# Performance work log

Measured on AMD Instinct MI355X. Metric: run time of the kernel, lower is better.

The kernel has to match this reference:

```python
import jax, jax.numpy as jnp
import numpy as np
from jax import lax

B, C, H, W = 8, 384, 32, 32
HEADS, G, STRIDE, KSIZE = 12, 6, 2, 3
HC = C // HEADS          # head channels = 32
CG = C // G              # group channels = 64
NGH = HEADS // G         # heads per group = 2
DEPTHS = 2
D2 = C * 4               # MLP hidden
HK, WK = H // STRIDE, W // STRIDE
NS = HK * WK             # deformable samples = 256
SCALE = HC ** -0.5


def dwconv(x, w, b, stride=1, pad=1):
    # depthwise conv, x:(N,Cx,H,W), w:(Cx,kh,kw)
    c = x.shape[1]
    y = lax.conv_general_dilated(x, w[:, None], (stride, stride),
                                 [(pad, pad), (pad, pad)], feature_group_count=c,
                                 dimension_numbers=('NCHW', 'OIHW', 'NCHW'))
    return y + b[None, :, None, None]


def conv1x1(x, w, b=None):
    y = jnp.einsum('oc,bchw->bohw', w, x)
    return y if b is None else y + b[None, :, None, None]


def layernorm_c(x, w, b, eps=1e-5):
    # LayerNormProxy: LN over channel dim of NCHW
    xt = x.transpose(0, 2, 3, 1)
    mu = xt.mean(-1, keepdims=True)
    var = xt.var(-1, keepdims=True)
    xt = (xt - mu) * lax.rsqrt(var + eps) * w + b
    return xt.transpose(0, 3, 1, 2)


def grid_sample(img, grid):
    # F.grid_sample, bilinear, align_corners=True. img:(N,Ci,Hi,Wi), grid:(N,Hg,Wg,2) as (x,y) in [-1,1]
    N, Ci, Hi, Wi = img.shape
    gx = (grid[..., 0] + 1.0) * 0.5 * (Wi - 1)
    gy = (grid[..., 1] + 1.0) * 0.5 * (Hi - 1)
    x0 = jnp.floor(gx)
    y0 = jnp.floor(gy)
    wx = (gx - x0)[:, None]   # (N,1,Hg,Wg)
    wy = (gy - y0)[:, None]
    x0i = jnp.clip(x0.astype(jnp.int32), 0, Wi - 1)
    y0i = jnp.clip(y0.astype(jnp.int32), 0, Hi - 1)
    x1i = jnp.clip(x0i + 1, 0, Wi - 1)
    y1i = jnp.clip(y0i + 1, 0, Hi - 1)
    gather = jax.vmap(lambda im, yi, xi: im[:, yi, xi])  # -> (N,Ci,Hg,Wg)
    v00 = gather(img, y0i, x0i)
    v01 = gather(img, y0i, x1i)
    v10 = gather(img, y1i, x0i)
    v11 = gather(img, y1i, x1i)
    return (v00 * (1 - wx) * (1 - wy) + v01 * wx * (1 - wy)
            + v10 * (1 - wx) * wy + v11 * wx * wy)


def _norm_grid(hs, ws, centered):
    if centered:  # _get_ref_points
        ys = jnp.linspace(0.5, hs - 0.5, hs)
        xs = jnp.linspace(0.5, ws - 0.5, ws)
    else:         # _get_q_grid
        ys = jnp.arange(hs, dtype=jnp.float32)
        xs = jnp.arange(ws, dtype=jnp.float32)
    ys = ys / (hs - 1.0) * 2.0 - 1.0
    xs = xs / (ws - 1.0) * 2.0 - 1.0
    return jnp.stack(jnp.meshgrid(ys, xs, indexing='ij'), -1)  # (hs,ws,2) (y,x)


def dattn(x, wq, bq, wk, bk, wv, bv, wo, bo, odw, odb, olw, olb, opw, rpe):
    q = conv1x1(x, wq, bq)                              # (B,C,H,W)
    q_off = q.reshape(B * G, CG, H, W)
    off = dwconv(q_off, odw, odb, stride=STRIDE, pad=KSIZE // 2)  # (BG,CG,HK,WK)
    off = jax.nn.gelu(layernorm_c(off, olw, olb), approximate=False)
    off = conv1x1(off, opw).transpose(0, 2, 3, 1)       # (BG,HK,WK,2) as (dy,dx)
    ref = _norm_grid(HK, WK, True)[None]
    pos = jnp.clip(off + ref, -1.0, 1.0)                # (BG,HK,WK,2) (y,x)
    xs = grid_sample(x.reshape(B * G, CG, H, W), pos[..., ::-1])  # (BG,CG,HK,WK)
    xs = xs.reshape(B, C, 1, NS)
    qf = q.reshape(B * HEADS, HC, H * W)
    k = conv1x1(xs, wk, bk).reshape(B * HEADS, HC, NS)
    v = conv1x1(xs, wv, bv).reshape(B * HEADS, HC, NS)
    attn = jnp.einsum('bcm,bcn->bmn', qf, k) * SCALE    # (B*HEADS, HW, NS)
    rpe_g = jnp.broadcast_to(rpe[None], (B,) + rpe.shape).reshape(B * G, NGH, 2 * H - 1, 2 * W - 1)
    qg = _norm_grid(H, W, False).reshape(1, H * W, 2)
    disp = (qg[:, :, None, :] - pos.reshape(B * G, 1, NS, 2)) * 0.5  # (BG,HW,NS,2)
    bias = grid_sample(rpe_g, disp[..., ::-1]).reshape(B * HEADS, H * W, NS)
    attn = jax.nn.softmax(attn + bias, axis=2)
    out = jnp.einsum('bmn,bcn->bcm', attn, v).reshape(B, C, H, W)
    return conv1x1(out, wo, bo)


def _forward(x, lpu_w, lpu_b, wq, bq, wk, bk, wv, bv, wo, bo,
             off_dw_w, off_dw_b, off_ln_w, off_ln_b, off_pw_w, rpe,
             mlp_w1, mlp_b1, mlp_dw_w, mlp_dw_b, mlp_w2, mlp_b2):
    # proj is Identity (dim_in == dim_embed); layer_norms/layer_scales/drop_path are Identity; dropouts are 0
    for d in range(DEPTHS):
        x = x + dwconv(x, lpu_w[d], lpu_b[d])  # local perception unit
        x = x + dattn(x, wq[d], bq[d], wk[d], bk[d], wv[d], bv[d], wo[d], bo[d],
                      off_dw_w[d], off_dw_b[d], off_ln_w[d], off_ln_b[d], off_pw_w[d], rpe[d])
        h = conv1x1(x, mlp_w1[d], mlp_b1[d])
        h = h + dwconv(h, mlp_dw_w[d], mlp_dw_b[d])
        h = jax.nn.gelu(h, approximate=False)
        x = x + conv1x1(h, mlp_w2[d], mlp_b2[d])
    return x


def setup_inputs():
    key = jax.random.key(0)
    ks = iter(jax.random.split(key, 16))
    def p(shape, std=0.02):
        return jax.random.normal(next(ks), shape, jnp.float32) * std
    D = DEPTHS
    return {
        "x": jax.random.normal(next(ks), (B, C, H, W), jnp.float32),
        "lpu_w": p((D, C, 3, 3)), "lpu_b": jnp.zeros((D, C), jnp.float32),
        "wq": p((D, C, C)), "bq": jnp.zeros((D, C), jnp.float32),
        "wk": p((D, C, C)), "bk": jnp.zeros((D, C), jnp.float32),
        "wv": p((D, C, C)), "bv": jnp.zeros((D, C), jnp.float32),
        "wo": p((D, C, C)), "bo": jnp.zeros((D, C), jnp.float32),
        "off_dw_w": p((D, CG, 3, 3)), "off_dw_b": jnp.zeros((D, CG), jnp.float32),
        "off_ln_w": jnp.ones((D, CG), jnp.float32), "off_ln_b": jnp.zeros((D, CG), jnp.float32),
        "off_pw_w": p((D, 2, CG)),
        "rpe": p((D, HEADS, 2 * H - 1, 2 * W - 1), 0.01),
        "mlp_w1": p((D, D2, C)), "mlp_b1": jnp.zeros((D, D2), jnp.float32),
        "mlp_dw_w": p((D, D2, 3, 3)), "mlp_dw_b": jnp.zeros((D, D2), jnp.float32),
        "mlp_w2": p((D, C, D2)), "mlp_b2": jnp.zeros((D, C), jnp.float32),
    }


def reference(x, lpu_w, lpu_b, wq, bq, wk, bk, wv, bv, wo, bo,
              off_dw_w, off_dw_b, off_ln_w, off_ln_b, off_pw_w, rpe,
              mlp_w1, mlp_b1, mlp_dw_w, mlp_dw_b, mlp_w2, mlp_b2):
    return _forward(x, lpu_w, lpu_b, wq, bq, wk, bk, wv, bv, wo, bo,
                    off_dw_w, off_dw_b, off_ln_w, off_ln_b, off_pw_w, rpe,
                    mlp_w1, mlp_b1, mlp_dw_w, mlp_dw_b, mlp_w2, mlp_b2)
```

## Files before the change

kernel.cpp:

```cpp
#include <hip/hip_runtime.h>
#include <hip/hip_bf16.h>
#include <math.h>

namespace {

constexpr int B_ = 8, C_ = 384, H_ = 32, W_ = 32, HW_ = 1024;
constexpr int HEADS_ = 12, G_ = 6, HC_ = 32, CG_ = 64, NS_ = 256, D2_ = 1536;
constexpr float SCALE_ = 0.17677669529663687f;

using short8 = __attribute__((ext_vector_type(8))) short;
using f32x4 = __attribute__((ext_vector_type(4))) float;
using u32x4 = __attribute__((ext_vector_type(4))) unsigned;
typedef unsigned short ushort_t;

__device__ __forceinline__ float gelu_exact(float x) {
  return 0.5f * x * (1.f + erff(x * 0.70710678118654752f));
}
__device__ __forceinline__ ushort_t f2bf(float f) {
  unsigned u = __float_as_uint(f);
  u = (u + 0x7FFFu + ((u >> 16) & 1u)) >> 16;
  return (ushort_t)u;
}
__device__ __forceinline__ float bf2f(ushort_t s) {
  return __uint_as_float(((unsigned)s) << 16);
}
__device__ __forceinline__ float bflo(unsigned u) { return __uint_as_float(u << 16); }
__device__ __forceinline__ float bfhi(unsigned u) { return __uint_as_float(u & 0xFFFF0000u); }
__device__ __forceinline__ unsigned pack2(float a, float b) {
  return (unsigned)f2bf(a) | ((unsigned)f2bf(b) << 16);
}

typedef __attribute__((address_space(1))) const unsigned int gq_u32;
typedef __attribute__((address_space(3))) unsigned int lq_u32;
__device__ __forceinline__ void gload16(const ushort_t* g, ushort_t* l) {
  __builtin_amdgcn_global_load_lds((gq_u32*)g, (lq_u32*)l, 16, 0, 0);
}

__global__ __launch_bounds__(256) void wcvt_kernel(
    const float* __restrict__ s0, const float* __restrict__ s1,
    const float* __restrict__ s2, const float* __restrict__ s3,
    const float* __restrict__ s4, const float* __restrict__ s5,
    ushort_t* __restrict__ dst) {
  long idx = (long)blockIdx.x * 256 + threadIdx.x;
  long off = idx;
  const float* s;
  if (off < 294912) s = s0;
  else if ((off -= 294912) < 294912) s = s1;
  else if ((off -= 294912) < 294912) s = s2;
  else if ((off -= 294912) < 294912) s = s3;
  else if ((off -= 294912) < 1179648) s = s4;
  else { off -= 1179648; s = s5; }
  dst[idx] = f2bf(s[off]);
}

__global__ __launch_bounds__(256) void rpe_pack(const float* __restrict__ rpe,
                                               uint2* __restrict__ rpq) {
  int h = blockIdx.x, d = blockIdx.y;
  const float* rph = rpe + ((size_t)d * HEADS_ + h) * 3969;
  uint2* dst = rpq + ((size_t)d * HEADS_ + h) * 4096;
  for (int i = threadIdx.x; i < 4096; i += 256) {
    int y = i >> 6, x = i & 63;
    float v00 = 0.f, v01 = 0.f, v10 = 0.f, v11 = 0.f;
    if (y < 63) {
      if (x < 63) v00 = rph[y * 63 + x];
      if (x < 62) v01 = rph[y * 63 + x + 1];
    }
    if (y < 62) {
      if (x < 63) v10 = rph[(y + 1) * 63 + x];
      if (x < 62) v11 = rph[(y + 1) * 63 + x + 1];
    }
    dst[i] = make_uint2(pack2(v00, v01), pack2(v10, v11));
  }
}

__global__ __launch_bounds__(256) void dwconv_lpu(
    const float* __restrict__ x, const float* __restrict__ w,
    const float* __restrict__ bias, float* __restrict__ y,
    ushort_t* __restrict__ yt) {
  __shared__ __align__(16) float tile[32][33];
  int hp = blockIdx.x, c0 = blockIdx.y * 32, b = blockIdx.z;
  int t = threadIdx.x;
  int cl = t >> 3, g4 = t & 7;
  int c = c0 + cl;
  const float* img = x + ((size_t)b * C_ + c) * HW_;
  const float* wc = w + c * 9;
  float o0 = bias[c], o1 = o0, o2 = o0, o3 = o0;
#pragma unroll
  for (int ky = 0; ky < 3; ++ky) {
    int ih = hp + ky - 1;
    if ((unsigned)ih >= 32u) continue;
    const float* row = img + ih * 32 + g4 * 4;
    float4 m = *(const float4*)row;
    float v0 = (g4 > 0) ? row[-1] : 0.f;
    float v5 = (g4 < 7) ? row[4] : 0.f;
    float k0 = wc[ky * 3], k1 = wc[ky * 3 + 1], k2 = wc[ky * 3 + 2];
    o0 = fmaf(k0, v0, fmaf(k1, m.x, fmaf(k2, m.y, o0)));
    o1 = fmaf(k0, m.x, fmaf(k1, m.y, fmaf(k2, m.z, o1)));
    o2 = fmaf(k0, m.y, fmaf(k1, m.z, fmaf(k2, m.w, o2)));
    o3 = fmaf(k0, m.z, fmaf(k1, m.w, fmaf(k2, v5, o3)));
  }
  float4 ctr = *(const float4*)(img + hp * 32 + g4 * 4);
  o0 += ctr.x; o1 += ctr.y; o2 += ctr.z; o3 += ctr.w;
  *(float4*)(y + ((size_t)b * C_ + c) * HW_ + hp * 32 + g4 * 4) =
      make_float4(o0, o1, o2, o3);
  tile[cl][g4 * 4 + 0] = o0;
  tile[cl][g4 * 4 + 1] = o1;
  tile[cl][g4 * 4 + 2] = o2;
  tile[cl][g4 * 4 + 3] = o3;
  __syncthreads();
  int wl = t >> 3, cg = t & 7;
  unsigned p0 = pack2(tile[cg * 4 + 0][wl], tile[cg * 4 + 1][wl]);
  unsigned p1 = pack2(tile[cg * 4 + 2][wl], tile[cg * 4 + 3][wl]);
  unsigned* dst = (unsigned*)(yt + ((size_t)b * HW_ + hp * 32 + wl) * C_ + c0 + cg * 4);
  dst[0] = p0;
  dst[1] = p1;
}

__global__ __launch_bounds__(256) void dwgelu_t(
    const ushort_t* __restrict__ hin, const float* __restrict__ w,
    const float* __restrict__ bias, ushort_t* __restrict__ ht) {
  __shared__ __align__(16) float tile[2][32][33];
  int hp0 = blockIdx.x * 2, c0 = blockIdx.y * 32, b = blockIdx.z;
  int t = threadIdx.x;
  int cl = t >> 3, rw = (t >> 2) & 1, g8 = t & 3;
  int hp = hp0 + rw;
  int c = c0 + cl;
  const ushort_t* img = hin + ((size_t)b * D2_ + c) * HW_;
  const float* wc = w + c * 9;
  float o[8];
  float bi = bias[c];
#pragma unroll
  for (int j = 0; j < 8; ++j) o[j] = bi;
#pragma unroll
  for (int ky = 0; ky < 3; ++ky) {
    int ih = hp + ky - 1;
    if ((unsigned)ih >= 32u) continue;
    const ushort_t* row = img + ih * 32 + g8 * 8;
    uint4 u = *(const uint4*)row;
    float vv[10];
    vv[0] = (g8 > 0) ? bf2f(row[-1]) : 0.f;
    vv[1] = bflo(u.x); vv[2] = bfhi(u.x); vv[3] = bflo(u.y); vv[4] = bfhi(u.y);
    vv[5] = bflo(u.z); vv[6] = bfhi(u.z); vv[7] = bflo(u.w); vv[8] = bfhi(u.w);
    vv[9] = (g8 < 3) ? bf2f(row[8]) : 0.f;
    float k0 = wc[ky * 3], k1 = wc[ky * 3 + 1], k2 = wc[ky * 3 + 2];
#pragma unroll
    for (int j = 0; j < 8; ++j)
      o[j] = fmaf(k0, vv[j], fmaf(k1, vv[j + 1], fmaf(k2, vv[j + 2], o[j])));
  }
  {
    uint4 u = *(const uint4*)(img + hp * 32 + g8 * 8);
    float cv[8] = {bflo(u.x), bfhi(u.x), bflo(u.y), bfhi(u.y),
                   bflo(u.z), bfhi(u.z), bflo(u.w), bfhi(u.w)};
#pragma unroll
    for (int j = 0; j < 8; ++j) {
      o[j] += cv[j];
      tile[rw][cl][g8 * 8 + j] = gelu_exact(o[j]);
    }
  }
  __syncthreads();
  int wl = t >> 3, cg = t & 7;
#pragma unroll
  for (int rr = 0; rr < 2; ++rr) {
    unsigned p0 = pack2(tile[rr][cg * 4 + 0][wl], tile[rr][cg * 4 + 1][wl]);
    unsigned p1 = pack2(tile[rr][cg * 4 + 2][wl], tile[rr][cg * 4 + 3][wl]);
    unsigned* dst = (unsigned*)(ht + ((size_t)b * HW_ + (hp0 + rr) * 32 + wl) * D2_ + c0 + cg * 4);
    dst[0] = p0;
    dst[1] = p1;
  }
}

__global__ __launch_bounds__(256) void gemm_kv(
    const ushort_t* __restrict__ Wk, const ushort_t* __restrict__ Wv,
    const ushort_t* __restrict__ Xt, const float* __restrict__ bk,
    const float* __restrict__ bv, ushort_t* __restrict__ ktb,
    ushort_t* __restrict__ vbn) {
  constexpr int K = C_, N = NS_, O = C_;
  struct __align__(16) SMem {
    union {
      struct { char a[8192]; char b[8192]; } st;
      float shuf[64 * 68];
    };
  };
  __shared__ SMem sm;
  int t = threadIdx.x;
  int lane = t & 63, wave = t >> 6;
  int wm = (wave >> 1) * 32, wn = (wave & 1) * 32;
  int bz = blockIdx.z;
  bool isK = blockIdx.y < 6;
  int o0 = (isK ? blockIdx.y : blockIdx.y - 6) * 64;
  int n0 = blockIdx.x * 64;
  const ushort_t* Wb = isK ? Wk : Wv;
  const float* bias = isK ? bk : bv;
  const ushort_t* Ag = Wb + (size_t)o0 * K;
  const ushort_t* Bg = Xt + ((size_t)bz * N + n0) * K;
  int sr = t >> 3, sc = t & 7;
  int swz = ((sc ^ (sr & 7)) << 4);
  f32x4 acc[2][2];
#pragma unroll
  for (int fi = 0; fi < 2; ++fi)
#pragma unroll
    for (int fj = 0; fj < 2; ++fj) acc[fi][fj] = f32x4{0.f, 0.f, 0.f, 0.f};
  int lrow = lane & 15, lk = lane >> 4;
  short8 a0 = *(const short8*)(Ag + (size_t)sr * K + sc * 8);
  short8 a1 = *(const short8*)(Ag + (size_t)(sr + 32) * K + sc * 8);
  short8 b0 = *(const short8*)(Bg + (size_t)sr * K + sc * 8);
  short8 b1 = *(const short8*)(Bg + (size_t)(sr + 32) * K + sc * 8);
  constexpr int NSTEP = K / 64;
#pragma unroll
  for (int s = 0; s < NSTEP; ++s) {
    if (s) __syncthreads();
    *(short8*)(sm.st.a + sr * 128 + swz) = a0;
    *(short8*)(sm.st.a + (sr + 32) * 128 + swz) = a1;
    *(short8*)(sm.st.b + sr * 128 + swz) = b0;
    *(short8*)(sm.st.b + (sr + 32) * 128 + swz) = b1;
    __syncthreads();
    if (s + 1 < NSTEP) {
      int k0 = (s + 1) * 64;
      a0 = *(const short8*)(Ag + (size_t)sr * K + k0 + sc * 8);
      a1 = *(const short8*)(Ag + (size_t)(sr + 32) * K + k0 + sc * 8);
      b0 = *(const short8*)(Bg + (size_t)sr * K + k0 + sc * 8);
      b1 = *(const short8*)(Bg + (size_t)(sr + 32) * K + k0 + sc * 8);
    }
#pragma unroll
    for (int kk = 0; kk < 2; ++kk) {
      short8 af[2], bfr[2];
#pragma unroll
      for (int fi = 0; fi < 2; ++fi) {
        int row = wm + fi * 16 + lrow;
        af[fi] = *(const short8*)(sm.st.a + row * 128 + (((kk * 4 + lk) ^ (row & 7)) << 4));
      }
#pragma unroll
      for (int fj = 0; fj < 2; ++fj) {
        int row = wn + fj * 16 + lrow;
        bfr[fj] = *(const short8*)(sm.st.b + row * 128 + (((kk * 4 + lk) ^ (row & 7)) << 4));
      }
#pragma unroll
      for (int fi = 0; fi < 2; ++fi)
#pragma unroll
        for (int fj = 0; fj < 2; ++fj)
          acc[fi][fj] = __builtin_amdgcn_mfma_f32_16x16x32_bf16(af[fi], bfr[fj], acc[fi][fj], 0, 0, 0);
    }
  }
  __syncthreads();
#pragma unroll
  for (int fi = 0; fi < 2; ++fi) {
#pragma unroll
    for (int r = 0; r < 4; ++r) {
      int ol = wm + fi * 16 + lk * 4 + r;
      float bi = bias[o0 + ol];
#pragma unroll
      for (int fj = 0; fj < 2; ++fj) {
        int nl = wn + fj * 16 + lrow;
        sm.shuf[ol * 68 + nl] = acc[fi][fj][r] + bi;
      }
    }
  }
  __syncthreads();
  if (isK) {
    int nl = t >> 2, og = (t & 3) * 16;
    unsigned pk[8];
#pragma unroll
    for (int i = 0; i < 8; ++i)
      pk[i] = pack2(sm.shuf[(og + 2 * i) * 68 + nl], sm.shuf[(og + 2 * i + 1) * 68 + nl]);
    unsigned* dst = (unsigned*)(ktb + ((size_t)bz * N + (n0 + nl)) * O + o0 + og);
    *(uint4*)(dst) = make_uint4(pk[0], pk[1], pk[2], pk[3]);
    *(uint4*)(dst + 4) = make_uint4(pk[4], pk[5], pk[6], pk[7]);
  } else {
    int ol = t >> 2, ng = (t & 3) * 16;
    unsigned pk[8];
#pragma unroll
    for (int i = 0; i < 8; ++i)
      pk[i] = pack2(sm.shuf[ol * 68 + ng + 2 * i], sm.shuf[ol * 68 + ng + 2 * i + 1]);
    unsigned* dst = (unsigned*)(vbn + ((size_t)bz * O + (o0 + ol)) * N + n0 + ng);
    *(uint4*)(dst) = make_uint4(pk[0], pk[1], pk[2], pk[3]);
    *(uint4*)(dst + 4) = make_uint4(pk[4], pk[5], pk[6], pk[7]);
  }
}

template <bool F32, bool B16N, bool B16T, bool RES>
__global__ __launch_bounds__(256) void gemm128(
    const ushort_t* __restrict__ Wb, const ushort_t* __restrict__ Xt,
    const float* __restrict__ bias, const float* __restrict__ resid,
    float* __restrict__ Y, ushort_t* __restrict__ Yb, int O, int K, int N) {
  __shared__ __align__(16) ushort_t sA[2][128 * 64];
  __shared__ __align__(16) ushort_t sB[2][128 * 64];
  int t = threadIdx.x;
  int l = t & 63, w = t >> 6;
  int o0 = blockIdx.y * 128, n0 = blockIdx.x * 128, bz = blockIdx.z;
  const ushort_t* Ag = Wb + (size_t)o0 * K;
  const ushort_t* Bg = Xt + ((size_t)bz * N + n0) * K;
  int srow = w * 32 + (l >> 3);
  int scol = (l & 7) * 8;
  int lrow = l & 15, lg = l >> 4;
  int wm = (w >> 1) * 64, wn = (w & 1) * 64;
  f32x4 acc[4][4];
#pragma unroll
  for (int fi = 0; fi < 4; ++fi)
#pragma unroll
    for (int fj = 0; fj < 4; ++fj) acc[fi][fj] = f32x4{0.f, 0.f, 0.f, 0.f};
  auto stage = [&](int buf, int k0) {
#pragma unroll
    for (int i = 0; i < 4; ++i) {
      gload16(Ag + (size_t)(srow + i * 8) * K + k0 + scol, sA[buf] + (w * 32 + i * 8) * 64);
      gload16(Bg + (size_t)(srow + i * 8) * K + k0 + scol, sB[buf] + (w * 32 + i * 8) * 64);
    }
  };
  stage(0, 0);
  __syncthreads();
  int nstep = K >> 6;
  for (int s = 0; s < nstep; ++s) {
    int cur = s & 1;
    if (s + 1 < nstep) stage(cur ^ 1, (s + 1) * 64);
#pragma unroll
    for (int kk = 0; kk < 2; ++kk) {
      short8 af[4], bfr[4];
#pragma unroll
      for (int fi = 0; fi < 4; ++fi)
        af[fi] = *(const short8*)(sA[cur] + (wm + fi * 16 + lrow) * 64 + kk * 32 + lg * 8);
#pragma unroll
      for (int fj = 0; fj < 4; ++fj)
        bfr[fj] = *(const short8*)(sB[cur] + (wn + fj * 16 + lrow) * 64 + kk * 32 + lg * 8);
#pragma unroll
      for (int fi = 0; fi < 4; ++fi)
#pragma unroll
        for (int fj = 0; fj < 4; ++fj)
          acc[fi][fj] = __builtin_amdgcn_mfma_f32_16x16x32_bf16(af[fi], bfr[fj], acc[fi][fj], 0, 0, 0);
    }
    __syncthreads();
  }
#pragma unroll
  for (int fi = 0; fi < 4; ++fi) {
    int ob = wm + fi * 16 + lg * 4;
    float bi[4];
#pragma unroll
    for (int r = 0; r < 4; ++r) bi[r] = bias[o0 + ob + r];
#pragma unroll
    for (int fj = 0; fj < 4; ++fj) {
      int n = n0 + wn + fj * 16 + lrow;
      float v[4];
#pragma unroll
      for (int r = 0; r < 4; ++r) {
        v[r] = acc[fi][fj][r] + bi[r];
        if (RES) v[r] += resid[((size_t)bz * O + ob + r + o0) * N + n];
        if (F32) Y[((size_t)bz * O + ob + r + o0) * N + n] = v[r];
        if (B16N) Yb[((size_t)bz * O + ob + r + o0) * N + n] = f2bf(v[r]);
      }
      if (B16T) {
        uint2 u;
        u.x = pack2(v[0], v[1]);
        u.y = pack2(v[2], v[3]);
        *(uint2*)&Yb[((size_t)bz * N + n) * O + o0 + ob] = u;
      }
    }
  }
}

__global__ __launch_bounds__(256) void offset_kernel(
    const ushort_t* __restrict__ qt, const float* __restrict__ odw,
    const float* __restrict__ odb, const float* __restrict__ olw,
    const float* __restrict__ olb, const float* __restrict__ opw,
    float* __restrict__ pos) {
  int bg = blockIdx.x;
  int b = bg / G_, g = bg % G_;
  int t = threadIdx.x;
  int hk = t >> 4, wk = t & 15;
  const ushort_t* qb = qt + (size_t)b * HW_ * C_ + g * CG_;
  float sv[CG_];
#pragma unroll
  for (int cc = 0; cc < 8; ++cc) {
    float a8[8];
#pragma unroll
    for (int j = 0; j < 8; ++j) a8[j] = odb[cc * 8 + j];
#pragma unroll
    for (int ky = 0; ky < 3; ++ky) {
      int ih = 2 * hk + ky - 1;
      if ((unsigned)ih >= 32u) continue;
#pragma unroll
      for (int kx = 0; kx < 3; ++kx) {
        int iw = 2 * wk + kx - 1;
        if ((unsigned)iw >= 32u) continue;
        uint4 u = *(const uint4*)(qb + (size_t)(ih * 32 + iw) * C_ + cc * 8);
        float vv[8] = {bflo(u.x), bfhi(u.x), bflo(u.y), bfhi(u.y),
                       bflo(u.z), bfhi(u.z), bflo(u.w), bfhi(u.w)};
#pragma unroll
        for (int j = 0; j < 8; ++j)
          a8[j] = fmaf(odw[(cc * 8 + j) * 9 + ky * 3 + kx], vv[j], a8[j]);
      }
    }
#pragma unroll
    for (int j = 0; j < 8; ++j) sv[cc * 8 + j] = a8[j];
  }
  float mu = 0.f;
#pragma unroll
  for (int c = 0; c < CG_; c++) mu += sv[c];
  mu *= (1.f / CG_);
  float var = 0.f;
#pragma unroll
  for (int c = 0; c < CG_; c++) {
    float d = sv[c] - mu;
    var = fmaf(d, d, var);
  }
  var *= (1.f / CG_);
  float rs = rsqrtf(var + 1e-5f);
  float dy = 0.f, dx = 0.f;
#pragma unroll
  for (int c = 0; c < CG_; c++) {
    float tv = (sv[c] - mu) * rs * olw[c] + olb[c];
    float ge = gelu_exact(tv);
    dy = fmaf(opw[c], ge, dy);
    dx = fmaf(opw[CG_ + c], ge, dx);
  }
  float ry = (hk + 0.5f) * (2.f / 15.f) - 1.f;
  float rx = (wk + 0.5f) * (2.f / 15.f) - 1.f;
  pos[(size_t)bg * 512 + t * 2 + 0] = fminf(fmaxf(dy + ry, -1.f), 1.f);
  pos[(size_t)bg * 512 + t * 2 + 1] = fminf(fmaxf(dx + rx, -1.f), 1.f);
}

__global__ __launch_bounds__(256) void sample_xst(
    const float* __restrict__ y1, const float* __restrict__ pos,
    ushort_t* __restrict__ xst) {
  int bg = blockIdx.y;
  int b = bg / G_, g = bg % G_;
  int t = threadIdx.x;
  int cg = t & 63, nl = t >> 6;
  int n = blockIdx.x * 4 + nl;
  float py = pos[(size_t)bg * 512 + 2 * n];
  float px = pos[(size_t)bg * 512 + 2 * n + 1];
  float gx = (px + 1.f) * 15.5f, gy = (py + 1.f) * 15.5f;
  float fx = floorf(gx), fy = floorf(gy);
  float wx = gx - fx, wy = gy - fy;
  int x0 = min(max((int)fx, 0), 31), y0 = min(max((int)fy, 0), 31);
  int x1 = min(x0 + 1, 31), y1i = min(y0 + 1, 31);
  const float* img = y1 + ((size_t)b * C_ + g * CG_ + cg) * HW_;
  float v00 = img[y0 * 32 + x0], v01 = img[y0 * 32 + x1];
  float v10 = img[y1i * 32 + x0], v11 = img[y1i * 32 + x1];
  float v = v00 * (1.f - wx) * (1.f - wy) + v01 * wx * (1.f - wy) +
            v10 * (1.f - wx) * wy + v11 * wx * wy;
  xst[((size_t)b * NS_ + n) * C_ + g * CG_ + cg] = f2bf(v);
}

__global__ __launch_bounds__(256) void attn_kernel(
    const ushort_t* __restrict__ qt, const ushort_t* __restrict__ kt,
    const ushort_t* __restrict__ vbn, const float* __restrict__ pos,
    const uint2* __restrict__ rpq, ushort_t* __restrict__ aot) {
  __shared__ __align__(16) uint2 sRPQ[4096];
  __shared__ __align__(16) ushort_t sP[4][32 * 40];
  __shared__ unsigned sIB[256];
  __shared__ float sW2[512];
  int bid = blockIdx.x;
  int swzb = (bid & 7) * 96 + (bid >> 3);
  int qb = swzb & 7;
  int grp = swzb >> 3;
  int h = grp % HEADS_;
  int b = grp / HEADS_;
  int t = threadIdx.x;
  int l = t & 63, wv = t >> 6;
  int lrow = l & 15, lg = l >> 4;
  int bg = b * G_ + (h >> 1);
  {
    const ushort_t* src = (const ushort_t*)(rpq + (size_t)h * 4096);
    ushort_t* dstb = (ushort_t*)sRPQ;
#pragma unroll
    for (int i = 0; i < 8; ++i)
      gload16(src + i * 2048 + t * 8, dstb + i * 2048 + wv * 512);
  }
  {
    float py = pos[(size_t)bg * 512 + 2 * t];
    float px = pos[(size_t)bg * 512 + 2 * t + 1];
    float cy = 15.5f - 15.5f * py;
    float cx = 15.5f - 15.5f * px;
    float fy = floorf(cy), fx = floorf(cx);
    sIB[t] = (unsigned)((int)fy * 64 + (int)fx);
    sW2[2 * t] = cy - fy;
    sW2[2 * t + 1] = cx - fx;
  }
  __syncthreads();

  int m0 = qb * 128 + wv * 32;
  short8 qf[2];
  int aq[2];
#pragma unroll
  for (int f = 0; f < 2; ++f) {
    int m = m0 + f * 16 + lrow;
    qf[f] = *(const short8*)(qt + ((size_t)b * HW_ + m) * C_ + h * HC_ + lg * 8);
    aq[f] = (m >> 5) * 64 + (m & 31);
  }
  const ushort_t* kbase = kt + (size_t)b * NS_ * C_ + h * HC_;
  const ushort_t* vbase = vbn + ((size_t)b * C_ + h * HC_) * NS_;
  f32x4 oc[2][2];
#pragma unroll
  for (int f = 0; f < 2; ++f)
#pragma unroll
    for (int ct = 0; ct < 2; ++ct) oc[f][ct] = f32x4{0.f, 0.f, 0.f, 0.f};
  float mrun[2] = {-1e30f, -1e30f}, lrun[2] = {0.f, 0.f};
  ushort_t* sPw = sP[wv];

  for (int c = 0; c < 8; ++c) {
    f32x4 s[2][2];
    __builtin_amdgcn_s_setprio(1);
#pragma unroll
    for (int T = 0; T < 2; ++T) {
      short8 kf = *(const short8*)(kbase + (size_t)((c * 2 + T) * 16 + lrow) * C_ + lg * 8);
#pragma unroll
      for (int f = 0; f < 2; ++f)
        s[f][T] = __builtin_amdgcn_mfma_f32_16x16x32_bf16(kf, qf[f], f32x4{0.f, 0.f, 0.f, 0.f}, 0, 0, 0);
    }
    __builtin_amdgcn_s_setprio(0);
    u32x4 ibT[2];
    f32x4 wA[2], wB[2];
#pragma unroll
    for (int T = 0; T < 2; ++T) {
      int kbase2 = c * 32 + T * 16 + lg * 4;
      ibT[T] = *(const u32x4*)&sIB[kbase2];
      wA[T] = *(const f32x4*)&sW2[2 * kbase2];
      wB[T] = *(const f32x4*)&sW2[2 * kbase2 + 4];
    }
#pragma unroll
    for (int f = 0; f < 2; ++f)
#pragma unroll
      for (int T = 0; T < 2; ++T)
#pragma unroll
        for (int r = 0; r < 4; ++r) {
          int a = aq[f] + (int)ibT[T][r];
          float wy = (r < 2) ? wA[T][(r & 1) * 2] : wB[T][(r & 1) * 2];
          float wx = (r < 2) ? wA[T][(r & 1) * 2 + 1] : wB[T][(r & 1) * 2 + 1];
          uint2 qd = sRPQ[a];
          float b00 = bflo(qd.x), b01 = bfhi(qd.x);
          float b10 = bflo(qd.y), b11 = bfhi(qd.y);
          float r0 = b00 + wx * (b01 - b00);
          float r1 = b10 + wx * (b11 - b10);
          s[f][T][r] = s[f][T][r] * SCALE_ + r0 + wy * (r1 - r0);
        }
#pragma unroll
    for (int f = 0; f < 2; ++f) {
      float mx = s[f][0][0];
#pragma unroll
      for (int T = 0; T < 2; ++T)
#pragma unroll
        for (int r = 0; r < 4; ++r) mx = fmaxf(mx, s[f][T][r]);
      mx = fmaxf(mx, __shfl_xor(mx, 16));
      mx = fmaxf(mx, __shfl_xor(mx, 32));
      float newm = fmaxf(mrun[f], mx);
      float fac = __expf(mrun[f] - newm);
      mrun[f] = newm;
      float ps = 0.f;
#pragma unroll
      for (int T = 0; T < 2; ++T)
#pragma unroll
        for (int r = 0; r < 4; ++r) {
          float p = __expf(s[f][T][r] - newm);
          s[f][T][r] = p;
          ps += p;
        }
      ps += __shfl_xor(ps, 16);
      ps += __shfl_xor(ps, 32);
      lrun[f] = lrun[f] * fac + ps;
#pragma unroll
      for (int ct = 0; ct < 2; ++ct)
#pragma unroll
        for (int r = 0; r < 4; ++r) oc[f][ct][r] *= fac;
#pragma unroll
      for (int T = 0; T < 2; ++T) {
        uint2 u;
        u.x = pack2(s[f][T][0], s[f][T][1]);
        u.y = pack2(s[f][T][2], s[f][T][3]);
        *(uint2*)&sPw[(f * 16 + lrow) * 40 + T * 16 + lg * 4] = u;
      }
    }
    short8 pa[2];
#pragma unroll
    for (int f = 0; f < 2; ++f)
      pa[f] = *(const short8*)&sPw[(f * 16 + lrow) * 40 + lg * 8];
    __builtin_amdgcn_s_setprio(1);
#pragma unroll
    for (int ct = 0; ct < 2; ++ct) {
      short8 vf = *(const short8*)(vbase + (size_t)(ct * 16 + lrow) * NS_ + c * 32 + lg * 8);
#pragma unroll
      for (int f = 0; f < 2; ++f)
        oc[f][ct] = __builtin_amdgcn_mfma_f32_16x16x32_bf16(pa[f], vf, oc[f][ct], 0, 0, 0);
    }
    __builtin_amdgcn_s_setprio(0);
  }
#pragma unroll
  for (int f = 0; f < 2; ++f) {
    float inv = 1.f / lrun[f];
    float invq[4];
#pragma unroll
    for (int r = 0; r < 4; ++r) invq[r] = __shfl(inv, lg * 4 + r);
#pragma unroll
    for (int ct = 0; ct < 2; ++ct)
#pragma unroll
      for (int r = 0; r < 4; ++r) {
        int m = m0 + f * 16 + lg * 4 + r;
        aot[((size_t)b * HW_ + m) * C_ + h * HC_ + ct * 16 + lrow] =
            f2bf(oc[f][ct][r] * invq[r]);
      }
  }
}

}

extern "C" void kernel_launch(void* const* d_in, const int* in_sizes, int n_in,
                              void* d_out, int out_size, void* d_ws,
                              size_t ws_size, hipStream_t stream) {
  const float* x_in = (const float*)d_in[0];
  const float* lpu_w = (const float*)d_in[1];
  const float* lpu_b = (const float*)d_in[2];
  const float* wq = (const float*)d_in[3];
  const float* bq = (const float*)d_in[4];
  const float* wk = (const float*)d_in[5];
  const float* bk = (const float*)d_in[6];
  const float* wv = (const float*)d_in[7];
  const float* bv = (const float*)d_in[8];
  const float* wo = (const float*)d_in[9];
  const float* bo = (const float*)d_in[10];
  const float* odw = (const float*)d_in[11];
  const float* odb = (const float*)d_in[12];
  const float* olw = (const float*)d_in[13];
  const float* olb = (const float*)d_in[14];
  const float* opw = (const float*)d_in[15];
  const float* rpe = (const float*)d_in[16];
  const float* w1 = (const float*)d_in[17];
  const float* b1 = (const float*)d_in[18];
  const float* mdw = (const float*)d_in[19];
  const float* mdb = (const float*)d_in[20];
  const float* w2 = (const float*)d_in[21];
  const float* b2 = (const float*)d_in[22];
  float* out = (float*)d_out;

  constexpr size_t XSZ = (size_t)B_ * C_ * HW_;
  constexpr size_t SSZ = (size_t)B_ * C_ * NS_;
  constexpr size_t HSZ = (size_t)B_ * D2_ * HW_;

  char* base = (char*)d_ws;
  auto alloc = [&](size_t bytes) {
    char* p = base;
    base += (bytes + 255) & ~(size_t)255;
    return p;
  };
  float* bufX = (float*)alloc(XSZ * 4);
  float* y1 = (float*)alloc(XSZ * 4);
  float* x2 = (float*)alloc(XSZ * 4);
  float* pos = (float*)alloc(48 * 512 * 4);
  ushort_t* qt = (ushort_t*)alloc(XSZ * 2);
  ushort_t* tb1 = (ushort_t*)alloc(XSZ * 2);
  ushort_t* aot = (ushort_t*)alloc(XSZ * 2);
  ushort_t* xst = (ushort_t*)alloc(SSZ * 2);
  ushort_t* ktb = (ushort_t*)alloc(SSZ * 2);
  ushort_t* vbn = (ushort_t*)alloc(SSZ * 2);
  ushort_t* h1b = (ushort_t*)alloc(HSZ * 2);
  ushort_t* h3t = (ushort_t*)alloc(HSZ * 2);
  ushort_t* wb = (ushort_t*)alloc((size_t)3538944 * 2);
  uint2* rpq = (uint2*)alloc((size_t)2 * HEADS_ * 4096 * 8);

  ushort_t* wqb = wb;
  ushort_t* wkb = wb + 294912;
  ushort_t* wvb = wb + 589824;
  ushort_t* wob = wb + 884736;
  ushort_t* w1b = wb + 1179648;
  ushort_t* w2b = wb + 2359296;

  wcvt_kernel<<<3538944 / 256, 256, 0, stream>>>(wq, wk, wv, wo, w1, w2, wb);
  rpe_pack<<<dim3(HEADS_, 2), 256, 0, stream>>>(rpe, rpq);

  for (int d = 0; d < 2; ++d) {
    const float* xin = (d == 0) ? x_in : bufX;
    float* xnext = (d == 1) ? out : bufX;
    const ushort_t* wqd = wqb + (size_t)d * 147456;
    const ushort_t* wkd = wkb + (size_t)d * 147456;
    const ushort_t* wvd = wvb + (size_t)d * 147456;
    const ushort_t* wod = wob + (size_t)d * 147456;
    const ushort_t* w1d = w1b + (size_t)d * 589824;
    const ushort_t* w2d = w2b + (size_t)d * 589824;

    dwconv_lpu<<<dim3(32, 12, 8), 256, 0, stream>>>(xin, lpu_w + d * C_ * 9,
                                                    lpu_b + d * C_, y1, tb1);
    gemm128<false, false, true, false><<<dim3(8, 3, 8), 256, 0, stream>>>(
        wqd, tb1, bq + d * C_, nullptr, nullptr, qt, C_, C_, HW_);
    offset_kernel<<<48, 256, 0, stream>>>(qt, odw + d * CG_ * 9, odb + d * CG_,
                                          olw + d * CG_, olb + d * CG_,
                                          opw + d * 2 * CG_, pos);
    sample_xst<<<dim3(64, 48), 256, 0, stream>>>(y1, pos, xst);
    gemm_kv<<<dim3(4, 12, 8), 256, 0, stream>>>(wkd, wvd, xst, bk + d * C_,
                                                bv + d * C_, ktb, vbn);
    attn_kernel<<<768, 256, 0, stream>>>(qt, ktb, vbn, pos,
                                         rpq + (size_t)d * HEADS_ * 4096, aot);
    gemm128<true, false, true, true><<<dim3(8, 3, 8), 256, 0, stream>>>(
        wod, aot, bo + d * C_, y1, x2, tb1, C_, C_, HW_);
    gemm128<false, true, false, false><<<dim3(8, 12, 8), 256, 0, stream>>>(
        w1d, tb1, b1 + d * D2_, nullptr, nullptr, h1b, D2_, C_, HW_);
    dwgelu_t<<<dim3(16, 48, 8), 256, 0, stream>>>(h1b, mdw + d * D2_ * 9,
                                                  mdb + d * D2_, h3t);
    gemm128<true, false, false, true><<<dim3(8, 3, 8), 256, 0, stream>>>(
        w2d, h3t, b2 + d * C_, x2, xnext, nullptr, C_, D2_, HW_);
  }
}
```

Before: 506.8 us.

## Fuse setup kernels, shrink N-tile for small GEMMs, split offset kernel, lazy softmax rescale

Merges the weight conversion and RPE packing into one launch. Adds a BN=64 variant of the GEMM for the O=384 projections, doubling block count to fill more CUs. The offset kernel now spreads each sample over four threads with shuffle reductions, giving 192 blocks instead of 48. Attention softmax skips the running-max rescale unless the new max exceeds the old one by more than 8, which saves exps and multiplies but lets exponent values grow up to e^8.

New measurement: 460.8 us. 1.1x faster.

```diff
diff --git a/kernel.cpp b/kernel.cpp
--- a/kernel.cpp
+++ b/kernel.cpp
@@ -36,40 +36,41 @@
   __builtin_amdgcn_global_load_lds((gq_u32*)g, (lq_u32*)l, 16, 0, 0);
 }
 
-__global__ __launch_bounds__(256) void wcvt_kernel(
+__global__ __launch_bounds__(256) void wcvt_rpe(
     const float* __restrict__ s0, const float* __restrict__ s1,
     const float* __restrict__ s2, const float* __restrict__ s3,
     const float* __restrict__ s4, const float* __restrict__ s5,
-    ushort_t* __restrict__ dst) {
-  long idx = (long)blockIdx.x * 256 + threadIdx.x;
-  long off = idx;
-  const float* s;
-  if (off < 294912) s = s0;
-  else if ((off -= 294912) < 294912) s = s1;
-  else if ((off -= 294912) < 294912) s = s2;
-  else if ((off -= 294912) < 294912) s = s3;
-  else if ((off -= 294912) < 1179648) s = s4;
-  else { off -= 1179648; s = s5; }
-  dst[idx] = f2bf(s[off]);
-}
-
-__global__ __launch_bounds__(256) void rpe_pack(const float* __restrict__ rpe,
-                                               uint2* __restrict__ rpq) {
-  int h = blockIdx.x, d = blockIdx.y;
-  const float* rph = rpe + ((size_t)d * HEADS_ + h) * 3969;
-  uint2* dst = rpq + ((size_t)d * HEADS_ + h) * 4096;
-  for (int i = threadIdx.x; i < 4096; i += 256) {
-    int y = i >> 6, x = i & 63;
-    float v00 = 0.f, v01 = 0.f, v10 = 0.f, v11 = 0.f;
-    if (y < 63) {
-      if (x < 63) v00 = rph[y * 63 + x];
-      if (x < 62) v01 = rph[y * 63 + x + 1];
-    }
-    if (y < 62) {
-      if (x < 63) v10 = rph[(y + 1) * 63 + x];
-      if (x < 62) v11 = rph[(y + 1) * 63 + x + 1];
-    }
-    dst[i] = make_uint2(pack2(v00, v01), pack2(v10, v11));
+    ushort_t* __restrict__ dst, const float* __restrict__ rpe,
+    uint2* __restrict__ rpq) {
+  int blk = blockIdx.x;
+  if (blk < 13824) {
+    long idx = (long)blk * 256 + threadIdx.x;
+    long off = idx;
+    const float* s;
+    if (off < 294912) s = s0;
+    else if ((off -= 294912) < 294912) s = s1;
+    else if ((off -= 294912) < 294912) s = s2;
+    else if ((off -= 294912) < 294912) s = s3;
+    else if ((off -= 294912) < 1179648) s = s4;
+    else { off -= 1179648; s = s5; }
+    dst[idx] = f2bf(s[off]);
+  } else {
+    int hb = blk - 13824;
+    const float* rph = rpe + (size_t)hb * 3969;
+    uint2* dq = rpq + (size_t)hb * 4096;
+    for (int i = threadIdx.x; i < 4096; i += 256) {
+      int y = i >> 6, x = i & 63;
+      float v00 = 0.f, v01 = 0.f, v10 = 0.f, v11 = 0.f;
+      if (y < 63) {
+        if (x < 63) v00 = rph[y * 63 + x];
+        if (x < 62) v01 = rph[y * 63 + x + 1];
+      }
+      if (y < 62) {
+        if (x < 63) v10 = rph[(y + 1) * 63 + x];
+        if (x < 62) v11 = rph[(y + 1) * 63 + x + 1];
+      }
+      dq[i] = make_uint2(pack2(v00, v01), pack2(v10, v11));
+    }
   }
 }
 
@@ -277,32 +278,44 @@
   }
 }
 
-template <bool F32, bool B16N, bool B16T, bool RES>
+template <int BN, bool F32, bool B16N, bool B16T, bool RES>
 __global__ __launch_bounds__(256) void gemm128(
     const ushort_t* __restrict__ Wb, const ushort_t* __restrict__ Xt,
     const float* __restrict__ bias, const float* __restrict__ resid,
     float* __restrict__ Y, ushort_t* __restrict__ Yb, int O, int K, int N) {
+  constexpr int MFW = (BN == 128) ? 4 : 2;
   __shared__ __align__(16) ushort_t sA[2][128 * 64];
-  __shared__ __align__(16) ushort_t sB[2][128 * 64];
+  __shared__ __align__(16) ushort_t sB[2][BN * 64];
   int t = threadIdx.x;
   int l = t & 63, w = t >> 6;
-  int o0 = blockIdx.y * 128, n0 = blockIdx.x * 128, bz = blockIdx.z;
+  int o0 = blockIdx.y * 128, n0 = blockIdx.x * BN, bz = blockIdx.z;
   const ushort_t* Ag = Wb + (size_t)o0 * K;
   const ushort_t* Bg = Xt + ((size_t)bz * N + n0) * K;
-  int srow = w * 32 + (l >> 3);
+  int lr8 = l >> 3;
   int scol = (l & 7) * 8;
   int lrow = l & 15, lg = l >> 4;
-  int wm = (w >> 1) * 64, wn = (w & 1) * 64;
-  f32x4 acc[4][4];
-#pragma unroll
-  for (int fi = 0; fi < 4; ++fi)
+  int wm = (BN == 128) ? (w >> 1) * 64 : w * 32;
+  int wn = (BN == 128) ? (w & 1) * 64 : 0;
+  f32x4 acc[MFW][4];
+#pragma unroll
+  for (int fi = 0; fi < MFW; ++fi)
 #pragma unroll
     for (int fj = 0; fj < 4; ++fj) acc[fi][fj] = f32x4{0.f, 0.f, 0.f, 0.f};
   auto stage = [&](int buf, int k0) {
 #pragma unroll
-    for (int i = 0; i < 4; ++i) {
-      gload16(Ag + (size_t)(srow + i * 8) * K + k0 + scol, sA[buf] + (w * 32 + i * 8) * 64);
-      gload16(Bg + (size_t)(srow + i * 8) * K + k0 + scol, sB[buf] + (w * 32 + i * 8) * 64);
+    for (int i = 0; i < 4; ++i)
+      gload16(Ag + (size_t)(w * 32 + i * 8 + lr8) * K + k0 + scol,
+              sA[buf] + (w * 32 + i * 8) * 64);
+    if constexpr (BN == 128) {
+#pragma unroll
+      for (int i = 0; i < 4; ++i)
+        gload16(Bg + (size_t)(w * 32 + i * 8 + lr8) * K + k0 + scol,
+                sB[buf] + (w * 32 + i * 8) * 64);
+    } else {
+#pragma unroll
+      for (int i = 0; i < 2; ++i)
+        gload16(Bg + (size_t)(w * 16 + i * 8 + lr8) * K + k0 + scol,
+                sB[buf] + (w * 16 + i * 8) * 64);
     }
   };
   stage(0, 0);
@@ -313,15 +326,15 @@
     if (s + 1 < nstep) stage(cur ^ 1, (s + 1) * 64);
 #pragma unroll
     for (int kk = 0; kk < 2; ++kk) {
-      short8 af[4], bfr[4];
-#pragma unroll
-      for (int fi = 0; fi < 4; ++fi)
+      short8 af[MFW], bfr[4];
+#pragma unroll
+      for (int fi = 0; fi < MFW; ++fi)
         af[fi] = *(const short8*)(sA[cur] + (wm + fi * 16 + lrow) * 64 + kk * 32 + lg * 8);
 #pragma unroll
       for (int fj = 0; fj < 4; ++fj)
         bfr[fj] = *(const short8*)(sB[cur] + (wn + fj * 16 + lrow) * 64 + kk * 32 + lg * 8);
 #pragma unroll
-      for (int fi = 0; fi < 4; ++fi)
+      for (int fi = 0; fi < MFW; ++fi)
 #pragma unroll
         for (int fj = 0; fj < 4; ++fj)
           acc[fi][fj] = __builtin_amdgcn_mfma_f32_16x16x32_bf16(af[fi], bfr[fj], acc[fi][fj], 0, 0, 0);
@@ -329,7 +342,7 @@
     __syncthreads();
   }
 #pragma unroll
-  for (int fi = 0; fi < 4; ++fi) {
+  for (int fi = 0; fi < MFW; ++fi) {
     int ob = wm + fi * 16 + lg * 4;
     float bi[4];
 #pragma unroll
@@ -360,60 +373,73 @@
     const float* __restrict__ odb, const float* __restrict__ olw,
     const float* __restrict__ olb, const float* __restrict__ opw,
     float* __restrict__ pos) {
-  int bg = blockIdx.x;
+  int blk = blockIdx.x;
+  int bg = blk >> 2, pb = blk & 3;
   int b = bg / G_, g = bg % G_;
   int t = threadIdx.x;
-  int hk = t >> 4, wk = t & 15;
-  const ushort_t* qb = qt + (size_t)b * HW_ * C_ + g * CG_;
-  float sv[CG_];
-#pragma unroll
-  for (int cc = 0; cc < 8; ++cc) {
-    float a8[8];
-#pragma unroll
-    for (int j = 0; j < 8; ++j) a8[j] = odb[cc * 8 + j];
-#pragma unroll
-    for (int ky = 0; ky < 3; ++ky) {
-      int ih = 2 * hk + ky - 1;
-      if ((unsigned)ih >= 32u) continue;
-#pragma unroll
-      for (int kx = 0; kx < 3; ++kx) {
-        int iw = 2 * wk + kx - 1;
-        if ((unsigned)iw >= 32u) continue;
-        uint4 u = *(const uint4*)(qb + (size_t)(ih * 32 + iw) * C_ + cc * 8);
-        float vv[8] = {bflo(u.x), bfhi(u.x), bflo(u.y), bfhi(u.y),
-                       bflo(u.z), bfhi(u.z), bflo(u.w), bfhi(u.w)};
-#pragma unroll
-        for (int j = 0; j < 8; ++j)
-          a8[j] = fmaf(odw[(cc * 8 + j) * 9 + ky * 3 + kx], vv[j], a8[j]);
-      }
-    }
-#pragma unroll
-    for (int j = 0; j < 8; ++j) sv[cc * 8 + j] = a8[j];
-  }
-  float mu = 0.f;
-#pragma unroll
-  for (int c = 0; c < CG_; c++) mu += sv[c];
-  mu *= (1.f / CG_);
-  float var = 0.f;
-#pragma unroll
-  for (int c = 0; c < CG_; c++) {
-    float d = sv[c] - mu;
-    var = fmaf(d, d, var);
-  }
-  var *= (1.f / CG_);
-  float rs = rsqrtf(var + 1e-5f);
+  int p = pb * 64 + (t >> 2);
+  int q = t & 3;
+  int c0 = q * 16;
+  int hk = p >> 4, wk = p & 15;
+  const ushort_t* qb = qt + (size_t)b * HW_ * C_ + g * CG_ + c0;
+  float sv[16];
+#pragma unroll
+  for (int j = 0; j < 16; ++j) sv[j] = odb[c0 + j];
+#pragma unroll
+  for (int ky = 0; ky < 3; ++ky) {
+    int ih = 2 * hk + ky - 1;
+    if ((unsigned)ih >= 32u) continue;
+#pragma unroll
+    for (int kx = 0; kx < 3; ++kx) {
+      int iw = 2 * wk + kx - 1;
+      if ((unsigned)iw >= 32u) continue;
+      const ushort_t* qp = qb + (size_t)(ih * 32 + iw) * C_;
+      uint4 u0 = *(const uint4*)qp;
+      uint4 u1 = *(const uint4*)(qp + 8);
+      float vv[16] = {bflo(u0.x), bfhi(u0.x), bflo(u0.y), bfhi(u0.y),
+                      bflo(u0.z), bfhi(u0.z), bflo(u0.w), bfhi(u0.w),
+                      bflo(u1.x), bfhi(u1.x), bflo(u1.y), bfhi(u1.y),
+                      bflo(u1.z), bfhi(u1.z), bflo(u1.w), bfhi(u1.w)};
+      int tap = ky * 3 + kx;
+#pragma unroll
+      for (int j = 0; j < 16; ++j)
+        sv[j] = fmaf(odw[(c0 + j) * 9 + tap], vv[j], sv[j]);
+    }
+  }
+  float s1 = 0.f;
+#pragma unroll
+  for (int j = 0; j < 16; ++j) s1 += sv[j];
+  s1 += __shfl_xor(s1, 1);
+  s1 += __shfl_xor(s1, 2);
+  float mu = s1 * (1.f / CG_);
+  float vs = 0.f;
+#pragma unroll
+  for (int j = 0; j < 16; ++j) {
+    float d = sv[j] - mu;
+    vs = fmaf(d, d, vs);
+  }
+  vs += __shfl_xor(vs, 1);
+  vs += __shfl_xor(vs, 2);
+  float rs = rsqrtf(vs * (1.f / CG_) + 1e-5f);
   float dy = 0.f, dx = 0.f;
 #pragma unroll
-  for (int c = 0; c < CG_; c++) {
-    float tv = (sv[c] - mu) * rs * olw[c] + olb[c];
+  for (int j = 0; j < 16; ++j) {
+    int c = c0 + j;
+    float tv = (sv[j] - mu) * rs * olw[c] + olb[c];
     float ge = gelu_exact(tv);
     dy = fmaf(opw[c], ge, dy);
     dx = fmaf(opw[CG_ + c], ge, dx);
   }
-  float ry = (hk + 0.5f) * (2.f / 15.f) - 1.f;
-  float rx = (wk + 0.5f) * (2.f / 15.f) - 1.f;
-  pos[(size_t)bg * 512 + t * 2 + 0] = fminf(fmaxf(dy + ry, -1.f), 1.f);
-  pos[(size_t)bg * 512 + t * 2 + 1] = fminf(fmaxf(dx + rx, -1.f), 1.f);
+  dy += __shfl_xor(dy, 1);
+  dy += __shfl_xor(dy, 2);
+  dx += __shfl_xor(dx, 1);
+  dx += __shfl_xor(dx, 2);
+  if (q == 0) {
+    float ry = (hk + 0.5f) * (2.f / 15.f) - 1.f;
+    float rx = (wk + 0.5f) * (2.f / 15.f) - 1.f;
+    pos[(size_t)bg * 512 + p * 2 + 0] = fminf(fmaxf(dy + ry, -1.f), 1.f);
+    pos[(size_t)bg * 512 + p * 2 + 1] = fminf(fmaxf(dx + rx, -1.f), 1.f);
+  }
 }
 
 __global__ __launch_bounds__(256) void sample_xst(
@@ -540,25 +566,28 @@
         for (int r = 0; r < 4; ++r) mx = fmaxf(mx, s[f][T][r]);
       mx = fmaxf(mx, __shfl_xor(mx, 16));
       mx = fmaxf(mx, __shfl_xor(mx, 32));
-      float newm = fmaxf(mrun[f], mx);
-      float fac = __expf(mrun[f] - newm);
-      mrun[f] = newm;
+      if (!__all(mx <= mrun[f] + 8.f)) {
+        float newm = fmaxf(mrun[f], mx);
+        float fac = __expf(mrun[f] - newm);
+        mrun[f] = newm;
+        lrun[f] *= fac;
+#pragma unroll
+        for (int ct = 0; ct < 2; ++ct)
+#pragma unroll
+          for (int r = 0; r < 4; ++r) oc[f][ct][r] *= fac;
+      }
       float ps = 0.f;
 #pragma unroll
       for (int T = 0; T < 2; ++T)
 #pragma unroll
         for (int r = 0; r < 4; ++r) {
-          float p = __expf(s[f][T][r] - newm);
+          float p = __expf(s[f][T][r] - mrun[f]);
           s[f][T][r] = p;
           ps += p;
         }
       ps += __shfl_xor(ps, 16);
       ps += __shfl_xor(ps, 32);
-      lrun[f] = lrun[f] * fac + ps;
-#pragma unroll
-      for (int ct = 0; ct < 2; ++ct)
-#pragma unroll
-        for (int r = 0; r < 4; ++r) oc[f][ct][r] *= fac;
+      lrun[f] += ps;
 #pragma unroll
       for (int T = 0; T < 2; ++T) {
         uint2 u;
@@ -660,8 +689,7 @@
   ushort_t* w1b = wb + 1179648;
   ushort_t* w2b = wb + 2359296;
 
-  wcvt_kernel<<<3538944 / 256, 256, 0, stream>>>(wq, wk, wv, wo, w1, w2, wb);
-  rpe_pack<<<dim3(HEADS_, 2), 256, 0, stream>>>(rpe, rpq);
+  wcvt_rpe<<<13824 + 24, 256, 0, stream>>>(wq, wk, wv, wo, w1, w2, wb, rpe, rpq);
 
   for (int d = 0; d < 2; ++d) {
     const float* xin = (d == 0) ? x_in : bufX;
@@ -675,23 +703,23 @@
 
     dwconv_lpu<<<dim3(32, 12, 8), 256, 0, stream>>>(xin, lpu_w + d * C_ * 9,
                                                     lpu_b + d * C_, y1, tb1);
-    gemm128<false, false, true, false><<<dim3(8, 3, 8), 256, 0, stream>>>(
+    gemm128<64, false, false, true, false><<<dim3(16, 3, 8), 256, 0, stream>>>(
         wqd, tb1, bq + d * C_, nullptr, nullptr, qt, C_, C_, HW_);
-    offset_kernel<<<48, 256, 0, stream>>>(qt, odw + d * CG_ * 9, odb + d * CG_,
-                                          olw + d * CG_, olb + d * CG_,
-                                          opw + d * 2 * CG_, pos);
+    offset_kernel<<<192, 256, 0, stream>>>(qt, odw + d * CG_ * 9, odb + d * CG_,
+                                           olw + d * CG_, olb + d * CG_,
+                                           opw + d * 2 * CG_, pos);
     sample_xst<<<dim3(64, 48), 256, 0, stream>>>(y1, pos, xst);
     gemm_kv<<<dim3(4, 12, 8), 256, 0, stream>>>(wkd, wvd, xst, bk + d * C_,
                                                 bv + d * C_, ktb, vbn);
     attn_kernel<<<768, 256, 0, stream>>>(qt, ktb, vbn, pos,
                                          rpq + (size_t)d * HEADS_ * 4096, aot);
-    gemm128<true, false, true, true><<<dim3(8, 3, 8), 256, 0, stream>>>(
+    gemm128<64, true, false, true, true><<<dim3(16, 3, 8), 256, 0, stream>>>(
         wod, aot, bo + d * C_, y1, x2, tb1, C_, C_, HW_);
-    gemm128<false, true, false, false><<<dim3(8, 12, 8), 256, 0, stream>>>(
+    gemm128<128, false, true, false, false><<<dim3(8, 12, 8), 256, 0, stream>>>(
         w1d, tb1, b1 + d * D2_, nullptr, nullptr, h1b, D2_, C_, HW_);
     dwgelu_t<<<dim3(16, 48, 8), 256, 0, stream>>>(h1b, mdw + d * D2_ * 9,
                                                   mdb + d * D2_, h3t);
-    gemm128<true, false, false, true><<<dim3(8, 3, 8), 256, 0, stream>>>(
+    gemm128<64, true, false, false, true><<<dim3(16, 3, 8), 256, 0, stream>>>(
         w2d, h3t, b2 + d * C_, x2, xnext, nullptr, C_, D2_, HW_);
   }
 }
```
